# Performance work log

Hardware: AMD Instinct MI355X
Metric: run time of the kernel (lower is better)

Reference implementation:

```python
import jax, jax.numpy as jnp
import numpy as np

N = 20000      # atoms
E = 320000     # directed edges
F = 128        # feat_dim
NRBF = 20
CUTOFF = 5.0
L = 3          # num_conv
EPS = 1e-15


def swish(x):
    return x * jax.nn.sigmoid(x)


def rbf(dist):
    # PainnRadialBasis: sin(n*pi*d/cutoff)/d, n = 1..NRBF
    n = jnp.arange(1, NRBF + 1, dtype=dist.dtype)
    d = dist[:, None]
    return jnp.sin(n * (jnp.pi / CUTOFF) * d) / d


def cos_envelope(dist):
    return jnp.where(dist < CUTOFF, 0.5 * (jnp.cos(jnp.pi * dist / CUTOFF) + 1.0), 0.0)


def vnorm(v):
    # NFF norm: sqrt(sum(v**2 + EPS))
    return jnp.sqrt(jnp.sum(v * v + EPS, axis=-1))


def setup_inputs() -> dict:
    key = jax.random.key(0)
    ks = jax.random.split(key, 32)
    s = 0.05
    inp = {
        'xyz': jax.random.uniform(ks[0], (N, 3), dtype=jnp.float32),
        'z': jax.random.randint(ks[1], (N,), 0, 100),
        'nbrs': jax.random.randint(ks[2], (E, 2), 0, N),
        # embedding + top-level DistEmb (n_rbf -> F)
        'embed_table': jax.random.normal(ks[3], (100, F), jnp.float32) * s,
        'de_w': jax.random.normal(ks[4], (NRBF, F), jnp.float32) * s,
        'de_b': jax.random.normal(ks[5], (F,), jnp.float32) * s,
        # message blocks (stacked over L layers)
        'msg_w1': jax.random.normal(ks[6], (L, F, F), jnp.float32) * s,
        'msg_b1': jax.random.normal(ks[7], (L, F), jnp.float32) * s,
        'msg_w2': jax.random.normal(ks[8], (L, F, 3 * F), jnp.float32) * s,
        'msg_b2': jax.random.normal(ks[9], (L, 3 * F), jnp.float32) * s,
        'msg_dw': jax.random.normal(ks[10], (L, NRBF, 3 * F), jnp.float32) * s,
        'msg_db': jax.random.normal(ks[11], (L, 3 * F), jnp.float32) * s,
        # update blocks
        'upd_u': jax.random.normal(ks[12], (L, F, F), jnp.float32) * s,
        'upd_v': jax.random.normal(ks[13], (L, F, F), jnp.float32) * s,
        'upd_w1': jax.random.normal(ks[14], (L, 2 * F, F), jnp.float32) * s,
        'upd_b1': jax.random.normal(ks[15], (L, F), jnp.float32) * s,
        'upd_w2': jax.random.normal(ks[16], (L, F, 3 * F), jnp.float32) * s,
        'upd_b2': jax.random.normal(ks[17], (L, 3 * F), jnp.float32) * s,
        # edge update MLPs
        'edge_w1': jax.random.normal(ks[18], (L, F, 2 * F), jnp.float32) * s,
        'edge_b1': jax.random.normal(ks[19], (L, 2 * F), jnp.float32) * s,
        'edge_w2': jax.random.normal(ks[20], (L, 2 * F, F), jnp.float32) * s,
        'edge_b2': jax.random.normal(ks[21], (L, F), jnp.float32) * s,
        # edge readout
        'ro_w1': jax.random.normal(ks[22], (F, 2 * F), jnp.float32) * s,
        'ro_b1': jax.random.normal(ks[23], (2 * F,), jnp.float32) * s,
        'ro_w2': jax.random.normal(ks[24], (2 * F, 1), jnp.float32) * s,
        'ro_b2': jax.random.normal(ks[25], (1,), jnp.float32) * s,
    }
    return inp


def forcepai_forward(xyz, embed_table, de_w, de_b, msg_w1, msg_b1, msg_w2, msg_b2,
                     msg_dw, msg_db, upd_u, upd_v, upd_w1, upd_b1, upd_w2, upd_b2,
                     edge_w1, edge_b1, edge_w2, edge_b2, ro_w1, ro_b1, ro_w2, ro_b2,
                     z, nbrs):
    seg = lambda x, idx: jax.ops.segment_sum(x, idx, num_segments=N)
    src, dst = nbrs[:, 0], nbrs[:, 1]

    r_ij = xyz[dst] - xyz[src]                       # (E, 3)
    dist = vnorm(r_ij)                               # (E,)
    unit = r_ij / dist[:, None]                      # (E, 3) == xyz_adjoint

    rbf_feats = rbf(dist)                            # (E, NRBF)
    env = cos_envelope(dist)[:, None]                # (E, 1)

    s_i = embed_table[z]                             # (N, F)
    v_i = jnp.zeros((N, F, 3), dtype=s_i.dtype)      # (N, F, 3)
    e_ij = (rbf_feats @ de_w + de_b) * env           # (E, F)

    for l in range(L):
        # --- MessageBlock ---
        phi = swish(s_i @ msg_w1[l] + msg_b1[l]) @ msg_w2[l] + msg_b2[l]   # (N, 3F)
        w_s = (rbf_feats @ msg_dw[l] + msg_db[l]) * env                    # (E, 3F)
        inv = (phi[dst] * w_s).reshape(E, 3, F)                            # (E, 3, F)
        split0 = inv[:, 0, :][..., None]                                   # (E, F, 1)
        split1 = inv[:, 1, :]                                              # (E, F)
        split2 = inv[:, 2, :][..., None]                                   # (E, F, 1)
        dv_ij = split2 * unit[:, None, :] + split0 * v_i[dst]              # (E, F, 3)
        s_i = s_i + seg(split1, src)
        v_i = v_i + seg(dv_ij, src)

        # --- UpdateBlock ---
        u_v = jnp.einsum('nfd,fg->ngd', v_i, upd_u[l])                     # (N, F, 3)
        v_v = jnp.einsum('nfd,fg->ngd', v_i, upd_v[l])                     # (N, F, 3)
        stack = jnp.concatenate([s_i, vnorm(v_v)], axis=-1)                # (N, 2F)
        split = (swish(stack @ upd_w1[l] + upd_b1[l]) @ upd_w2[l] + upd_b2[l]).reshape(N, 3, F)
        a_vv = split[:, 0, :][..., None]
        a_sv = split[:, 1, :]
        a_ss = split[:, 2, :]
        v_i = v_i + u_v * a_vv
        s_i = s_i + jnp.sum(u_v * v_v, axis=-1) * a_sv + a_ss

        # --- edge update ---
        pair = s_i[src] + s_i[dst]                                         # (E, F)
        e_ij = e_ij + (swish(pair @ edge_w1[l] + edge_b1[l]) @ edge_w2[l] + edge_b2[l])

    f_edge = (swish(e_ij @ ro_w1 + ro_b1) @ ro_w2 + ro_b2) * unit          # (E, 3)
    f_atom = seg(f_edge, src) - seg(f_edge, dst)                           # (N, 3)
    return f_atom


def reference(xyz, z, nbrs, embed_table, de_w, de_b, msg_w1, msg_b1, msg_w2, msg_b2,
              msg_dw, msg_db, upd_u, upd_v, upd_w1, upd_b1, upd_w2, upd_b2,
              edge_w1, edge_b1, edge_w2, edge_b2, ro_w1, ro_b1, ro_w2, ro_b2):
    return forcepai_forward(xyz, embed_table, de_w, de_b, msg_w1, msg_b1, msg_w2, msg_b2,
                            msg_dw, msg_db, upd_u, upd_v, upd_w1, upd_b1, upd_w2, upd_b2,
                            edge_w1, edge_b1, edge_w2, edge_b2, ro_w1, ro_b1, ro_w2, ro_b2,
                            z, nbrs)
```

## Files before the change

### kernel.cpp

```cpp
#include <hip/hip_runtime.h>

#define NA 20000
#define NE 320000
#define FD 128
#define NRBF 20
#define NL 3
#define PI_F 3.14159265358979323846f

typedef __attribute__((ext_vector_type(8))) short bf16x8;
typedef __attribute__((ext_vector_type(4))) float f32x4;

__device__ float g_unitv[NE*3];
__device__ float g_env[NE];
__device__ float g_rbf[NE*NRBF];
__device__ float g_s[NA*FD];
__device__ float g_vA[NA*3*FD];
__device__ float g_vB[NA*3*FD];
__device__ float g_phi[NA*3*FD];
__device__ float g_vv[NA*3*FD];
__device__ float g_stk[NA*2*FD];
__device__ float g_hsm[NA*FD];
__device__ int   g_off[NA+1];
__device__ int   g_cur[NA];
__device__ int   g_eid[NE];
__device__ unsigned short g_sb[NL*NA*FD];
__device__ unsigned short g_w1p[NL*FD*2*FD];
__device__ unsigned short g_w2p[NL*2*FD*FD];
__device__ unsigned short g_rw1p[FD*2*FD];
__device__ unsigned short g_mw1h[NL*FD*FD],   g_mw1l[NL*FD*FD];
__device__ unsigned short g_mw2h[NL*FD*3*FD], g_mw2l[NL*FD*3*FD];
__device__ unsigned short g_uuh[NL*FD*FD],    g_uul[NL*FD*FD];
__device__ unsigned short g_uvh[NL*FD*FD],    g_uvl[NL*FD*FD];
__device__ unsigned short g_uw1h[NL*2*FD*FD], g_uw1l[NL*2*FD*FD];
__device__ unsigned short g_uw2h[NL*FD*3*FD], g_uw2l[NL*FD*3*FD];

__device__ __forceinline__ float swishf(float x) { return x / (1.0f + __expf(-x)); }
__device__ __forceinline__ unsigned short f2bf(float x) {
    unsigned int u = __float_as_uint(x);
    unsigned int r = (u + 0x7FFFu + ((u >> 16) & 1u)) >> 16;
    return (unsigned short)r;
}
__device__ __forceinline__ float bf2f(unsigned short u) {
    return __uint_as_float(((unsigned int)u) << 16);
}

__global__ __launch_bounds__(256) void k_geom(const float* __restrict__ xyz, const int* __restrict__ nbrs)
{
    int e = blockIdx.x * 256 + threadIdx.x;
    if (e >= NE) return;
    int si = nbrs[2*e], di = nbrs[2*e+1];
    float rx = xyz[3*di+0] - xyz[3*si+0];
    float ry = xyz[3*di+1] - xyz[3*si+1];
    float rz = xyz[3*di+2] - xyz[3*si+2];
    float d2 = rx*rx + ry*ry + rz*rz + 3e-15f;
    float dist = sqrtf(d2);
    float inv = 1.0f / dist;
    g_unitv[3*e+0] = rx*inv;
    g_unitv[3*e+1] = ry*inv;
    g_unitv[3*e+2] = rz*inv;
    g_env[e] = (dist < 5.0f) ? 0.5f*(cosf(PI_F*dist*0.2f) + 1.0f) : 0.0f;
    #pragma unroll
    for (int k = 0; k < NRBF; ++k)
        g_rbf[(size_t)e*NRBF + k] = sinf((float)(k+1) * (PI_F*0.2f) * dist) * inv;
}

__global__ __launch_bounds__(256) void k_embed(const int* __restrict__ z, const float* __restrict__ table)
{
    int idx = blockIdx.x * 256 + threadIdx.x;
    if (idx >= NA * FD) return;
    int n = idx >> 7, f = idx & 127;
    g_s[idx] = table[z[n]*FD + f];
}

__global__ __launch_bounds__(256) void k_zero(float* __restrict__ fout)
{
    int idx = blockIdx.x * 256 + threadIdx.x;
    if (idx < NA*3*FD) g_vA[idx] = 0.f;
    if (idx < NA)      g_cur[idx] = 0;
    if (idx < NA*3)    fout[idx] = 0.f;
}

__global__ __launch_bounds__(256) void k_snap(int l)
{
    int idx = blockIdx.x * 256 + threadIdx.x;
    if (idx < NA*FD) g_sb[(size_t)l*NA*FD + idx] = f2bf(g_s[idx]);
}

__global__ __launch_bounds__(256) void k_pack(const float* __restrict__ W, unsigned short* __restrict__ out,
                                              int K, int N)
{
    int idx = blockIdx.x * 256 + threadIdx.x;
    int total = (K >> 5) * (N >> 4) * 64;
    if (idx >= total) return;
    int lane = idx & 63;
    int kc = (idx >> 6) % (K >> 5);
    int nt = (idx >> 6) / (K >> 5);
    int col = nt*16 + (lane & 15);
    int kb  = kc*32 + (lane >> 4) * 8;
    bf16x8 v;
    #pragma unroll
    for (int j = 0; j < 8; ++j) v[j] = (short)f2bf(W[(size_t)(kb + j) * N + col]);
    *reinterpret_cast<bf16x8*>(out + (size_t)idx * 8) = v;
}

__global__ __launch_bounds__(256) void k_pack_split(const float* __restrict__ W,
        unsigned short* __restrict__ hi, unsigned short* __restrict__ lo, int K, int N)
{
    int idx = blockIdx.x * 256 + threadIdx.x;
    int total = (K >> 5) * (N >> 4) * 64;
    if (idx >= total) return;
    int lane = idx & 63;
    int kc = (idx >> 6) % (K >> 5);
    int nt = (idx >> 6) / (K >> 5);
    int col = nt*16 + (lane & 15);
    int kb  = kc*32 + (lane >> 4) * 8;
    bf16x8 vh, vl;
    #pragma unroll
    for (int j = 0; j < 8; ++j) {
        float wv = W[(size_t)(kb + j) * N + col];
        unsigned short h = f2bf(wv);
        vh[j] = (short)h;
        vl[j] = (short)f2bf(wv - bf2f(h));
    }
    *reinterpret_cast<bf16x8*>(hi + (size_t)idx * 8) = vh;
    *reinterpret_cast<bf16x8*>(lo + (size_t)idx * 8) = vl;
}

__global__ __launch_bounds__(256) void k_count(const int* __restrict__ nbrs)
{
    int e = blockIdx.x * 256 + threadIdx.x;
    if (e < NE) atomicAdd(&g_cur[nbrs[2*e]], 1);
}

__global__ __launch_bounds__(1024) void k_scan()
{
    __shared__ int sd[1024];
    __shared__ int sbase;
    int tid = threadIdx.x;
    if (tid == 0) sbase = 0;
    __syncthreads();
    for (int c0 = 0; c0 < NA; c0 += 1024) {
        int i = c0 + tid;
        int x = (i < NA) ? g_cur[i] : 0;
        sd[tid] = x;
        __syncthreads();
        for (int o = 1; o < 1024; o <<= 1) {
            int t = (tid >= o) ? sd[tid - o] : 0;
            __syncthreads();
            sd[tid] += t;
            __syncthreads();
        }
        if (i < NA) { int excl = sbase + sd[tid] - x; g_off[i] = excl; g_cur[i] = excl; }
        __syncthreads();
        if (tid == 0) sbase += sd[1023];
        __syncthreads();
    }
    if (tid == 0) g_off[NA] = sbase;
}

__global__ __launch_bounds__(256) void k_fill(const int* __restrict__ nbrs)
{
    int e = blockIdx.x * 256 + threadIdx.x;
    if (e < NE) { int p = atomicAdd(&g_cur[nbrs[2*e]], 1); g_eid[p] = e; }
}

template<bool SWISH, int K, int N>
__global__ __launch_bounds__(256) void k_ngemm(const float* __restrict__ A,
        const unsigned short* __restrict__ Wh, const unsigned short* __restrict__ Wl,
        const float* __restrict__ bias, float* __restrict__ C, int R)
{
    constexpr int KCN = K >> 5;
    constexpr int NTN = N >> 4;
    int tid = threadIdx.x;
    int lane = tid & 63, w = tid >> 6;
    int r0 = blockIdx.x * 64 + w * 16;
    int arow = r0 + (lane & 15);
    int crow = r0 + ((lane >> 4) << 2);
    int ccol = lane & 15;

    bf16x8 ah[KCN], al[KCN];
    #pragma unroll
    for (int kc = 0; kc < KCN; ++kc) {
        float4 v0 = make_float4(0.f,0.f,0.f,0.f), v1 = make_float4(0.f,0.f,0.f,0.f);
        if (arow < R) {
            const float* ap = A + (size_t)arow*K + kc*32 + (lane >> 4)*8;
            v0 = *reinterpret_cast<const float4*>(ap);
            v1 = *reinterpret_cast<const float4*>(ap + 4);
        }
        float xv[8] = {v0.x, v0.y, v0.z, v0.w, v1.x, v1.y, v1.z, v1.w};
        #pragma unroll
        for (int j = 0; j < 8; ++j) {
            unsigned short h = f2bf(xv[j]);
            ah[kc][j] = (short)h;
            al[kc][j] = (short)f2bf(xv[j] - bf2f(h));
        }
    }
    #pragma unroll 4
    for (int nt = 0; nt < NTN; ++nt) {
        f32x4 acc = f32x4{0.f,0.f,0.f,0.f};
        #pragma unroll
        for (int kc = 0; kc < KCN; ++kc) {
            size_t fo = ((size_t)(nt*KCN + kc)*64 + lane)*8;
            bf16x8 wh = *reinterpret_cast<const bf16x8*>(Wh + fo);
            bf16x8 wl = *reinterpret_cast<const bf16x8*>(Wl + fo);
            acc = __builtin_amdgcn_mfma_f32_16x16x32_bf16(ah[kc], wh, acc, 0, 0, 0);
            acc = __builtin_amdgcn_mfma_f32_16x16x32_bf16(al[kc], wh, acc, 0, 0, 0);
            acc = __builtin_amdgcn_mfma_f32_16x16x32_bf16(ah[kc], wl, acc, 0, 0, 0);
        }
        int col = nt*16 + ccol;
        float bb = bias ? bias[col] : 0.f;
        #pragma unroll
        for (int i = 0; i < 4; ++i) {
            int row = crow + i;
            if (row < R) {
                float x = acc[i] + bb;
                C[(size_t)row*N + col] = SWISH ? swishf(x) : x;
            }
        }
    }
}

__global__ __launch_bounds__(128) void k_msg(
        const int* __restrict__ nbrs,
        const float* __restrict__ dw, const float* __restrict__ db,
        const float* __restrict__ vold, float* __restrict__ vnew)
{
    int n = blockIdx.x;
    int f = threadIdx.x;
    float sacc = 0.f, va0 = 0.f, va1 = 0.f, va2 = 0.f;
    int b = g_off[n], eend = g_off[n+1];
    float db0 = db[f], db1 = db[FD + f], db2 = db[2*FD + f];
    for (int ii = b; ii < eend; ++ii) {
        int e = g_eid[ii];
        int dst = nbrs[2*e+1];
        float ev = g_env[e];
        float rb[NRBF];
        const float4* rp = reinterpret_cast<const float4*>(g_rbf + (size_t)e*NRBF);
        #pragma unroll
        for (int q = 0; q < 5; ++q) { float4 t = rp[q]; rb[4*q]=t.x; rb[4*q+1]=t.y; rb[4*q+2]=t.z; rb[4*q+3]=t.w; }
        float w0 = db0, w1 = db1, w2 = db2;
        #pragma unroll
        for (int k = 0; k < NRBF; ++k) {
            float r = rb[k];
            w0 = fmaf(r, dw[k*3*FD + f],        w0);
            w1 = fmaf(r, dw[k*3*FD + FD + f],   w1);
            w2 = fmaf(r, dw[k*3*FD + 2*FD + f], w2);
        }
        w0 *= ev; w1 *= ev; w2 *= ev;
        const float* pd = g_phi + (size_t)dst*3*FD;
        float p0 = pd[f]        * w0;
        float p1 = pd[FD + f]   * w1;
        float p2 = pd[2*FD + f] * w2;
        sacc += p1;
        float ux = g_unitv[3*e+0], uy = g_unitv[3*e+1], uz = g_unitv[3*e+2];
        const float* vd = vold + (size_t)dst*3*FD;
        va0 = fmaf(p2, ux, fmaf(p0, vd[f],        va0));
        va1 = fmaf(p2, uy, fmaf(p0, vd[FD + f],   va1));
        va2 = fmaf(p2, uz, fmaf(p0, vd[2*FD + f], va2));
    }
    size_t nb = (size_t)n*3*FD;
    vnew[nb + f]        = vold[nb + f]        + va0;
    vnew[nb + FD + f]   = vold[nb + FD + f]   + va1;
    vnew[nb + 2*FD + f] = vold[nb + 2*FD + f] + va2;
    g_s[n*FD + f] += sacc;
}

__global__ __launch_bounds__(256) void k_stack()
{
    int idx = blockIdx.x * 256 + threadIdx.x;
    if (idx >= NA * FD) return;
    int n = idx >> 7, f = idx & 127;
    const float* v = g_vv + (size_t)n*3*FD;
    float a = v[f], b = v[FD + f], c = v[2*FD + f];
    float vn = sqrtf(a*a + b*b + c*c + 3e-15f);
    g_stk[(size_t)n*2*FD + f]      = g_s[idx];
    g_stk[(size_t)n*2*FD + FD + f] = vn;
}

__global__ __launch_bounds__(256) void k_apply(const float* __restrict__ split, float* __restrict__ v)
{
    int idx = blockIdx.x * 256 + threadIdx.x;
    if (idx >= NA * FD) return;
    int n = idx >> 7, f = idx & 127;
    const float* sp = split + (size_t)n*3*FD;
    float avv = sp[f], asv = sp[FD + f], ass = sp[2*FD + f];
    size_t nb = (size_t)n*3*FD;
    float dot = 0.f;
    #pragma unroll
    for (int d = 0; d < 3; ++d) {
        float u = g_phi[nb + d*FD + f], w = g_vv[nb + d*FD + f];
        v[nb + d*FD + f] += u * avv;
        dot = fmaf(u, w, dot);
    }
    g_s[idx] += dot * asv + ass;
}

__global__ __launch_bounds__(256) void k_edge_fused(
        const int* __restrict__ nbrs,
        const float* __restrict__ de_w, const float* __restrict__ de_b,
        const float* __restrict__ eb1, const float* __restrict__ eb2,
        const float* __restrict__ ro_b1, const float* __restrict__ ro_w2,
        const float* __restrict__ ro_b2, float* __restrict__ fatom)
{
    __shared__ unsigned short pairA[64*128];
    __shared__ unsigned short hid[64*256];
    __shared__ int nbrL[128];
    int tid = threadIdx.x;
    int e0 = blockIdx.x * 64;

    float* rbfL  = reinterpret_cast<float*>(pairA);
    float* envL  = rbfL + 64*NRBF;
    float* de_wL = reinterpret_cast<float*>(hid);

    if (tid < 128) nbrL[tid] = nbrs[2*e0 + tid];
    #pragma unroll
    for (int i = 0; i < 5; ++i) {
        int j = i*256 + tid;
        if (j < 64*NRBF) rbfL[j] = g_rbf[(size_t)e0*NRBF + j];
    }
    if (tid < 64) envL[tid] = g_env[e0 + tid];
    #pragma unroll
    for (int i = 0; i < 10; ++i) {
        int j = i*256 + tid;
        de_wL[j] = de_w[j];
    }
    __syncthreads();

    int lane = tid & 63, w = tid >> 6;
    int r0 = w * 16;
    int arow = r0 + (lane & 15);
    int crow = r0 + ((lane >> 4) << 2);
    int ccol = lane & 15;

    f32x4 acc_e[8];
    #pragma unroll
    for (int nt = 0; nt < 8; ++nt) acc_e[nt] = f32x4{0.f, 0.f, 0.f, 0.f};
    #pragma unroll 4
    for (int k = 0; k < NRBF; ++k) {
        float rb[4];
        #pragma unroll
        for (int i = 0; i < 4; ++i) rb[i] = rbfL[(crow + i)*NRBF + k];
        #pragma unroll
        for (int nt = 0; nt < 8; ++nt) {
            float wv = de_wL[k*FD + nt*16 + ccol];
            #pragma unroll
            for (int i = 0; i < 4; ++i) acc_e[nt][i] = fmaf(rb[i], wv, acc_e[nt][i]);
        }
    }
    #pragma unroll
    for (int nt = 0; nt < 8; ++nt) {
        float bb = de_b[nt*16 + ccol];
        #pragma unroll
        for (int i = 0; i < 4; ++i) acc_e[nt][i] = (acc_e[nt][i] + bb) * envL[crow + i];
    }

    for (int l = 0; l < NL; ++l) {
        __syncthreads();
        const unsigned short* sb = g_sb + (size_t)l*NA*FD;
        #pragma unroll
        for (int i = 0; i < 4; ++i) {
            int idx = i*256 + tid;
            int r = idx >> 4, c8 = idx & 15;
            int si = nbrL[2*r], di = nbrL[2*r+1];
            bf16x8 a = *reinterpret_cast<const bf16x8*>(sb + (size_t)si*FD + c8*8);
            bf16x8 b = *reinterpret_cast<const bf16x8*>(sb + (size_t)di*FD + c8*8);
            bf16x8 v;
            #pragma unroll
            for (int j = 0; j < 8; ++j)
                v[j] = (short)f2bf(bf2f((unsigned short)a[j]) + bf2f((unsigned short)b[j]));
            int byte = (r*256 + c8*16) ^ ((r & 7) << 4);
            *reinterpret_cast<bf16x8*>(reinterpret_cast<char*>(pairA) + byte) = v;
        }
        __syncthreads();

        const unsigned short* w1l = g_w1p + (size_t)l*FD*2*FD;
        const unsigned short* w2l = g_w2p + (size_t)l*2*FD*FD;
        const float* b1l = eb1 + (size_t)l*2*FD;
        const float* b2l = eb2 + (size_t)l*FD;

        bf16x8 a1f[4];
        #pragma unroll
        for (int kc = 0; kc < 4; ++kc) {
            int byte = (arow*256 + kc*64 + (lane >> 4)*16) ^ ((arow & 7) << 4);
            a1f[kc] = *reinterpret_cast<const bf16x8*>(reinterpret_cast<const char*>(pairA) + byte);
        }
        #pragma unroll 4
        for (int nt = 0; nt < 16; ++nt) {
            f32x4 acc = f32x4{0.f, 0.f, 0.f, 0.f};
            #pragma unroll
            for (int kc = 0; kc < 4; ++kc) {
                bf16x8 bv = *reinterpret_cast<const bf16x8*>(w1l + ((size_t)(nt*4 + kc)*64 + lane)*8);
                acc = __builtin_amdgcn_mfma_f32_16x16x32_bf16(a1f[kc], bv, acc, 0, 0, 0);
            }
            int col = nt*16 + ccol;
            float bb = b1l[col];
            #pragma unroll
            for (int i = 0; i < 4; ++i) {
                int row = crow + i;
                float h = swishf(acc[i] + bb);
                int byte = (row*512 + col*2) ^ ((row & 7) << 4);
                *reinterpret_cast<unsigned short*>(reinterpret_cast<char*>(hid) + byte) = f2bf(h);
            }
        }
        bf16x8 a2f[8];
        #pragma unroll
        for (int kc = 0; kc < 8; ++kc) {
            int byte = (arow*512 + kc*64 + (lane >> 4)*16) ^ ((arow & 7) << 4);
            a2f[kc] = *reinterpret_cast<const bf16x8*>(reinterpret_cast<const char*>(hid) + byte);
        }
        #pragma unroll 4
        for (int nt = 0; nt < 8; ++nt) {
            f32x4 acc = acc_e[nt];
            #pragma unroll
            for (int kc = 0; kc < 8; ++kc) {
                bf16x8 bv = *reinterpret_cast<const bf16x8*>(w2l + ((size_t)(nt*8 + kc)*64 + lane)*8);
                acc = __builtin_amdgcn_mfma_f32_16x16x32_bf16(a2f[kc], bv, acc, 0, 0, 0);
            }
            float bb = b2l[nt*16 + ccol];
            #pragma unroll
            for (int i = 0; i < 4; ++i) acc[i] += bb;
            acc_e[nt] = acc;
        }
    }

    #pragma unroll
    for (int nt = 0; nt < 8; ++nt) {
        int col = nt*16 + ccol;
        #pragma unroll
        for (int i = 0; i < 4; ++i) {
            int row = crow + i;
            int byte = (row*256 + col*2) ^ ((row & 7) << 4);
            *reinterpret_cast<unsigned short*>(reinterpret_cast<char*>(pairA) + byte) = f2bf(acc_e[nt][i]);
        }
    }
    bf16x8 a1f[4];
    #pragma unroll
    for (int kc = 0; kc < 4; ++kc) {
        int byte = (arow*256 + kc*64 + (lane >> 4)*16) ^ ((arow & 7) << 4);
        a1f[kc] = *reinterpret_cast<const bf16x8*>(reinterpret_cast<const char*>(pairA) + byte);
    }
    #pragma unroll 4
    for (int nt = 0; nt < 16; ++nt) {
        f32x4 acc = f32x4{0.f, 0.f, 0.f, 0.f};
        #pragma unroll
        for (int kc = 0; kc < 4; ++kc) {
            bf16x8 bv = *reinterpret_cast<const bf16x8*>(g_rw1p + ((size_t)(nt*4 + kc)*64 + lane)*8);
            acc = __builtin_amdgcn_mfma_f32_16x16x32_bf16(a1f[kc], bv, acc, 0, 0, 0);
        }
        int col = nt*16 + ccol;
        float bb = ro_b1[col];
        #pragma unroll
        for (int i = 0; i < 4; ++i) {
            int row = crow + i;
            float h = swishf(acc[i] + bb);
            int byte = (row*512 + col*2) ^ ((row & 7) << 4);
            *reinterpret_cast<unsigned short*>(reinterpret_cast<char*>(hid) + byte) = f2bf(h);
        }
    }
    int erow = r0 + (lane >> 2);
    int kp = lane & 3;
    float part = 0.f;
    #pragma unroll
    for (int cc = 0; cc < 8; ++cc) {
        int byte = (erow*512 + kp*128 + cc*16) ^ ((erow & 7) << 4);
        bf16x8 hv = *reinterpret_cast<const bf16x8*>(reinterpret_cast<const char*>(hid) + byte);
        const float* wp = ro_w2 + kp*64 + cc*8;
        #pragma unroll
        for (int j = 0; j < 8; ++j)
            part = fmaf(bf2f((unsigned short)hv[j]), wp[j], part);
    }
    part += __shfl_xor(part, 1);
    part += __shfl_xor(part, 2);
    if (kp == 0) {
        int e = e0 + erow;
        float sc = part + ro_b2[0];
        int si = nbrL[2*erow], di = nbrL[2*erow+1];
        #pragma unroll
        for (int d = 0; d < 3; ++d) {
            float fe = sc * g_unitv[3*e+d];
            atomicAdd(&fatom[3*si+d], fe);
            atomicAdd(&fatom[3*di+d], -fe);
        }
    }
}

extern "C" void kernel_launch(void* const* d_in, const int* in_sizes, int n_in,
                              void* d_out, int out_size, void* d_ws, size_t ws_size,
                              hipStream_t stream)
{
    (void)in_sizes; (void)n_in; (void)out_size; (void)d_ws; (void)ws_size;
    const float* xyz    = (const float*)d_in[0];
    const int*   z      = (const int*)  d_in[1];
    const int*   nbrs   = (const int*)  d_in[2];
    const float* emb    = (const float*)d_in[3];
    const float* de_w   = (const float*)d_in[4];
    const float* de_b   = (const float*)d_in[5];
    const float* msg_w1 = (const float*)d_in[6];
    const float* msg_b1 = (const float*)d_in[7];
    const float* msg_w2 = (const float*)d_in[8];
    const float* msg_b2 = (const float*)d_in[9];
    const float* msg_dw = (const float*)d_in[10];
    const float* msg_db = (const float*)d_in[11];
    const float* upd_u  = (const float*)d_in[12];
    const float* upd_v  = (const float*)d_in[13];
    const float* upd_w1 = (const float*)d_in[14];
    const float* upd_b1 = (const float*)d_in[15];
    const float* upd_w2 = (const float*)d_in[16];
    const float* upd_b2 = (const float*)d_in[17];
    const float* edge_w1= (const float*)d_in[18];
    const float* edge_b1= (const float*)d_in[19];
    const float* edge_w2= (const float*)d_in[20];
    const float* edge_b2= (const float*)d_in[21];
    const float* ro_w1  = (const float*)d_in[22];
    const float* ro_b1  = (const float*)d_in[23];
    const float* ro_w2  = (const float*)d_in[24];
    const float* ro_b2  = (const float*)d_in[25];
    float* fout = (float*)d_out;

    void *pv;
    auto sym = [&](const void* s) { hipGetSymbolAddress(&pv, s); return pv; };
    float* vA  = (float*)sym(HIP_SYMBOL(g_vA));
    float* vB  = (float*)sym(HIP_SYMBOL(g_vB));
    float* phi = (float*)sym(HIP_SYMBOL(g_phi));
    float* vv  = (float*)sym(HIP_SYMBOL(g_vv));
    float* stk = (float*)sym(HIP_SYMBOL(g_stk));
    float* hsm = (float*)sym(HIP_SYMBOL(g_hsm));
    float* sft = (float*)sym(HIP_SYMBOL(g_s));
    unsigned short* w1p  = (unsigned short*)sym(HIP_SYMBOL(g_w1p));
    unsigned short* w2p  = (unsigned short*)sym(HIP_SYMBOL(g_w2p));
    unsigned short* rw1p = (unsigned short*)sym(HIP_SYMBOL(g_rw1p));
    unsigned short* mw1h = (unsigned short*)sym(HIP_SYMBOL(g_mw1h));
    unsigned short* mw1l = (unsigned short*)sym(HIP_SYMBOL(g_mw1l));
    unsigned short* mw2h = (unsigned short*)sym(HIP_SYMBOL(g_mw2h));
    unsigned short* mw2l = (unsigned short*)sym(HIP_SYMBOL(g_mw2l));
    unsigned short* uuh  = (unsigned short*)sym(HIP_SYMBOL(g_uuh));
    unsigned short* uul  = (unsigned short*)sym(HIP_SYMBOL(g_uul));
    unsigned short* uvh  = (unsigned short*)sym(HIP_SYMBOL(g_uvh));
    unsigned short* uvl  = (unsigned short*)sym(HIP_SYMBOL(g_uvl));
    unsigned short* uw1h = (unsigned short*)sym(HIP_SYMBOL(g_uw1h));
    unsigned short* uw1l = (unsigned short*)sym(HIP_SYMBOL(g_uw1l));
    unsigned short* uw2h = (unsigned short*)sym(HIP_SYMBOL(g_uw2h));
    unsigned short* uw2l = (unsigned short*)sym(HIP_SYMBOL(g_uw2l));

    auto packGrid = [](int K, int N) { return ((K >> 5) * (N >> 4) * 64 + 255) / 256; };

    k_zero <<<(NA*3*FD+255)/256, 256, 0, stream>>>(fout);
    k_geom <<<(NE+255)/256, 256, 0, stream>>>(xyz, nbrs);
    k_embed<<<(NA*FD+255)/256, 256, 0, stream>>>(z, emb);
    k_count<<<(NE+255)/256, 256, 0, stream>>>(nbrs);
    k_scan <<<1, 1024, 0, stream>>>();
    k_fill <<<(NE+255)/256, 256, 0, stream>>>(nbrs);
    for (int l = 0; l < NL; ++l) {
        k_pack<<<packGrid(FD,2*FD), 256, 0, stream>>>(edge_w1 + (size_t)l*FD*2*FD, w1p + (size_t)l*FD*2*FD, FD, 2*FD);
        k_pack<<<packGrid(2*FD,FD), 256, 0, stream>>>(edge_w2 + (size_t)l*2*FD*FD, w2p + (size_t)l*2*FD*FD, 2*FD, FD);
        k_pack_split<<<packGrid(FD,FD),   256, 0, stream>>>(msg_w1 + (size_t)l*FD*FD,   mw1h + (size_t)l*FD*FD,   mw1l + (size_t)l*FD*FD,   FD, FD);
        k_pack_split<<<packGrid(FD,3*FD), 256, 0, stream>>>(msg_w2 + (size_t)l*FD*3*FD, mw2h + (size_t)l*FD*3*FD, mw2l + (size_t)l*FD*3*FD, FD, 3*FD);
        k_pack_split<<<packGrid(FD,FD),   256, 0, stream>>>(upd_u  + (size_t)l*FD*FD,   uuh  + (size_t)l*FD*FD,   uul  + (size_t)l*FD*FD,   FD, FD);
        k_pack_split<<<packGrid(FD,FD),   256, 0, stream>>>(upd_v  + (size_t)l*FD*FD,   uvh  + (size_t)l*FD*FD,   uvl  + (size_t)l*FD*FD,   FD, FD);
        k_pack_split<<<packGrid(2*FD,FD), 256, 0, stream>>>(upd_w1 + (size_t)l*2*FD*FD, uw1h + (size_t)l*2*FD*FD, uw1l + (size_t)l*2*FD*FD, 2*FD, FD);
        k_pack_split<<<packGrid(FD,3*FD), 256, 0, stream>>>(upd_w2 + (size_t)l*FD*3*FD, uw2h + (size_t)l*FD*3*FD, uw2l + (size_t)l*FD*3*FD, FD, 3*FD);
    }
    k_pack<<<packGrid(FD,2*FD), 256, 0, stream>>>(ro_w1, rw1p, FD, 2*FD);

    const int gN  = (NA + 63) / 64;
    const int g3N = (3*NA + 63) / 64;
    for (int l = 0; l < NL; ++l) {
        float* vOld = (l & 1) ? vB : vA;
        float* vNew = (l & 1) ? vA : vB;
        const float* mb1 = msg_b1 + (size_t)l*FD;
        const float* mb2 = msg_b2 + (size_t)l*3*FD;
        const float* mdw = msg_dw + (size_t)l*NRBF*3*FD;
        const float* mdb = msg_db + (size_t)l*3*FD;
        const float* ub1 = upd_b1 + (size_t)l*FD;
        const float* ub2 = upd_b2 + (size_t)l*3*FD;

        k_ngemm<true,128,128> <<<gN, 256, 0, stream>>>(sft, mw1h + (size_t)l*FD*FD, mw1l + (size_t)l*FD*FD, mb1, hsm, NA);
        k_ngemm<false,128,384><<<gN, 256, 0, stream>>>(hsm, mw2h + (size_t)l*FD*3*FD, mw2l + (size_t)l*FD*3*FD, mb2, phi, NA);
        k_msg<<<NA, FD, 0, stream>>>(nbrs, mdw, mdb, vOld, vNew);
        k_ngemm<false,128,128><<<g3N, 256, 0, stream>>>(vNew, uuh + (size_t)l*FD*FD, uul + (size_t)l*FD*FD, nullptr, phi, 3*NA);
        k_ngemm<false,128,128><<<g3N, 256, 0, stream>>>(vNew, uvh + (size_t)l*FD*FD, uvl + (size_t)l*FD*FD, nullptr, vv, 3*NA);
        k_stack<<<(NA*FD+255)/256, 256, 0, stream>>>();
        k_ngemm<true,256,128> <<<gN, 256, 0, stream>>>(stk, uw1h + (size_t)l*2*FD*FD, uw1l + (size_t)l*2*FD*FD, ub1, hsm, NA);
        k_ngemm<false,128,384><<<gN, 256, 0, stream>>>(hsm, uw2h + (size_t)l*FD*3*FD, uw2l + (size_t)l*FD*3*FD, ub2, vOld , NA);
        k_apply<<<(NA*FD+255)/256, 256, 0, stream>>>(vOld, vNew);
        k_snap<<<(NA*FD+255)/256, 256, 0, stream>>>(l);
    }
    k_edge_fused<<<NE/64, 256, 0, stream>>>(nbrs, de_w, de_b, edge_b1, edge_b2,
                                            ro_b1, ro_w2, ro_b2, fout);
}
```

Baseline: 2.435 ms.

## Split edge MLP hidden into halves and fuse readout dot into MFMA epilogue

The edge-update MLP now computes the 256-wide hidden layer in two 128-column halves. Each half is consumed immediately by the second GEMM, which halves the hidden shared-memory buffer. The readout's final 256->1 projection is folded into the first readout GEMM epilogue as per-lane FMAs followed by a cross-lane shuffle reduction, so the hidden activations are no longer written to and re-read from LDS. Less LDS per block may raise occupancy, but the extra accumulation in registers and the wider shuffle reduction add register pressure and instructions.

```diff
diff --git a/kernel.cpp b/kernel.cpp
--- a/kernel.cpp
+++ b/kernel.cpp
@@ -303,7 +303,7 @@
         const float* __restrict__ ro_b2, float* __restrict__ fatom)
 {
     __shared__ unsigned short pairA[64*128];
-    __shared__ unsigned short hid[64*256];
+    __shared__ unsigned short hid[64*128];
     __shared__ int nbrL[128];
     int tid = threadIdx.x;
     int e0 = blockIdx.x * 64;
@@ -384,42 +384,45 @@
             int byte = (arow*256 + kc*64 + (lane >> 4)*16) ^ ((arow & 7) << 4);
             a1f[kc] = *reinterpret_cast<const bf16x8*>(reinterpret_cast<const char*>(pairA) + byte);
         }
-        #pragma unroll 4
-        for (int nt = 0; nt < 16; ++nt) {
-            f32x4 acc = f32x4{0.f, 0.f, 0.f, 0.f};
+        #pragma unroll
+        for (int half = 0; half < 2; ++half) {
             #pragma unroll
-            for (int kc = 0; kc < 4; ++kc) {
-                bf16x8 bv = *reinterpret_cast<const bf16x8*>(w1l + ((size_t)(nt*4 + kc)*64 + lane)*8);
-                acc = __builtin_amdgcn_mfma_f32_16x16x32_bf16(a1f[kc], bv, acc, 0, 0, 0);
+            for (int nt2 = 0; nt2 < 8; ++nt2) {
+                int nt = half*8 + nt2;
+                f32x4 acc = f32x4{0.f, 0.f, 0.f, 0.f};
+                #pragma unroll
+                for (int kc = 0; kc < 4; ++kc) {
+                    bf16x8 bv = *reinterpret_cast<const bf16x8*>(w1l + ((size_t)(nt*4 + kc)*64 + lane)*8);
+                    acc = __builtin_amdgcn_mfma_f32_16x16x32_bf16(a1f[kc], bv, acc, 0, 0, 0);
+                }
+                int col = nt*16 + ccol;
+                float bb = b1l[col];
+                int colh = col - half*128;
+                #pragma unroll
+                for (int i = 0; i < 4; ++i) {
+                    int row = crow + i;
+                    float h = swishf(acc[i] + bb);
+                    int byte = (row*256 + colh*2) ^ ((row & 7) << 4);
+                    *reinterpret_cast<unsigned short*>(reinterpret_cast<char*>(hid) + byte) = f2bf(h);
+                }
             }
-            int col = nt*16 + ccol;
-            float bb = b1l[col];
             #pragma unroll
-            for (int i = 0; i < 4; ++i) {
-                int row = crow + i;
-                float h = swishf(acc[i] + bb);
-                int byte = (row*512 + col*2) ^ ((row & 7) << 4);
-                *reinterpret_cast<unsigned short*>(reinterpret_cast<char*>(hid) + byte) = f2bf(h);
+            for (int kc2 = 0; kc2 < 4; ++kc2) {
+                int byte = (arow*256 + kc2*64 + (lane >> 4)*16) ^ ((arow & 7) << 4);
+                bf16x8 a2 = *reinterpret_cast<const bf16x8*>(reinterpret_cast<const char*>(hid) + byte);
+                int kc = half*4 + kc2;
+                #pragma unroll
+                for (int nt2 = 0; nt2 < 8; ++nt2) {
+                    bf16x8 bv = *reinterpret_cast<const bf16x8*>(w2l + ((size_t)(nt2*8 + kc)*64 + lane)*8);
+                    acc_e[nt2] = __builtin_amdgcn_mfma_f32_16x16x32_bf16(a2, bv, acc_e[nt2], 0, 0, 0);
+                }
             }
         }
-        bf16x8 a2f[8];
-        #pragma unroll
-        for (int kc = 0; kc < 8; ++kc) {
-            int byte = (arow*512 + kc*64 + (lane >> 4)*16) ^ ((arow & 7) << 4);
-            a2f[kc] = *reinterpret_cast<const bf16x8*>(reinterpret_cast<const char*>(hid) + byte);
-        }
-        #pragma unroll 4
-        for (int nt = 0; nt < 8; ++nt) {
-            f32x4 acc = acc_e[nt];
+        #pragma unroll
+        for (int nt2 = 0; nt2 < 8; ++nt2) {
+            float bb = b2l[nt2*16 + ccol];
             #pragma unroll
-            for (int kc = 0; kc < 8; ++kc) {
-                bf16x8 bv = *reinterpret_cast<const bf16x8*>(w2l + ((size_t)(nt*8 + kc)*64 + lane)*8);
-                acc = __builtin_amdgcn_mfma_f32_16x16x32_bf16(a2f[kc], bv, acc, 0, 0, 0);
-            }
-            float bb = b2l[nt*16 + ccol];
-            #pragma unroll
-            for (int i = 0; i < 4; ++i) acc[i] += bb;
-            acc_e[nt] = acc;
+            for (int i = 0; i < 4; ++i) acc_e[nt2][i] += bb;
         }
     }
 
@@ -430,56 +433,47 @@
         for (int i = 0; i < 4; ++i) {
             int row = crow + i;
             int byte = (row*256 + col*2) ^ ((row & 7) << 4);
-            *reinterpret_cast<unsigned short*>(reinterpret_cast<char*>(pairA) + byte) = f2bf(acc_e[nt][i]);
-        }
-    }
-    bf16x8 a1f[4];
+            *reinterpret_cast<unsigned short*>(reinterpret_cast<char*>(hid) + byte) = f2bf(acc_e[nt][i]);
+        }
+    }
+    bf16x8 af[4];
     #pragma unroll
     for (int kc = 0; kc < 4; ++kc) {
         int byte = (arow*256 + kc*64 + (lane >> 4)*16) ^ ((arow & 7) << 4);
-        a1f[kc] = *reinterpret_cast<const bf16x8*>(reinterpret_cast<const char*>(pairA) + byte);
-    }
+        af[kc] = *reinterpret_cast<const bf16x8*>(reinterpret_cast<const char*>(hid) + byte);
+    }
+    float part[4] = {0.f, 0.f, 0.f, 0.f};
     #pragma unroll 4
     for (int nt = 0; nt < 16; ++nt) {
         f32x4 acc = f32x4{0.f, 0.f, 0.f, 0.f};
         #pragma unroll
         for (int kc = 0; kc < 4; ++kc) {
             bf16x8 bv = *reinterpret_cast<const bf16x8*>(g_rw1p + ((size_t)(nt*4 + kc)*64 + lane)*8);
-            acc = __builtin_amdgcn_mfma_f32_16x16x32_bf16(a1f[kc], bv, acc, 0, 0, 0);
+            acc = __builtin_amdgcn_mfma_f32_16x16x32_bf16(af[kc], bv, acc, 0, 0, 0);
         }
         int col = nt*16 + ccol;
         float bb = ro_b1[col];
+        float wv = ro_w2[col];
+        #pragma unroll
+        for (int i = 0; i < 4; ++i) part[i] = fmaf(swishf(acc[i] + bb), wv, part[i]);
+    }
+    #pragma unroll
+    for (int m = 1; m < 16; m <<= 1) {
+        #pragma unroll
+        for (int i = 0; i < 4; ++i) part[i] += __shfl_xor(part[i], m);
+    }
+    if (ccol == 0) {
         #pragma unroll
         for (int i = 0; i < 4; ++i) {
-            int row = crow + i;
-            float h = swishf(acc[i] + bb);
-            int byte = (row*512 + col*2) ^ ((row & 7) << 4);
-            *reinterpret_cast<unsigned short*>(reinterpret_cast<char*>(hid) + byte) = f2bf(h);
-        }
-    }
-    int erow = r0 + (lane >> 2);
-    int kp = lane & 3;
-    float part = 0.f;
-    #pragma unroll
-    for (int cc = 0; cc < 8; ++cc) {
-        int byte = (erow*512 + kp*128 + cc*16) ^ ((erow & 7) << 4);
-        bf16x8 hv = *reinterpret_cast<const bf16x8*>(reinterpret_cast<const char*>(hid) + byte);
-        const float* wp = ro_w2 + kp*64 + cc*8;
-        #pragma unroll
-        for (int j = 0; j < 8; ++j)
-            part = fmaf(bf2f((unsigned short)hv[j]), wp[j], part);
-    }
-    part += __shfl_xor(part, 1);
-    part += __shfl_xor(part, 2);
-    if (kp == 0) {
-        int e = e0 + erow;
-        float sc = part + ro_b2[0];
-        int si = nbrL[2*erow], di = nbrL[2*erow+1];
-        #pragma unroll
-        for (int d = 0; d < 3; ++d) {
-            float fe = sc * g_unitv[3*e+d];
-            atomicAdd(&fatom[3*si+d], fe);
-            atomicAdd(&fatom[3*di+d], -fe);
+            int e = e0 + crow + i;
+            float sc = part[i] + ro_b2[0];
+            int si = nbrL[2*(crow+i)], di = nbrL[2*(crow+i)+1];
+            #pragma unroll
+            for (int d = 0; d < 3; ++d) {
+                float fe = sc * g_unitv[3*e+d];
+                atomicAdd(&fatom[3*si+d], fe);
+                atomicAdd(&fatom[3*di+d], -fe);
+            }
         }
     }
 }
```

After: 2.896 ms. 18.9% more time.
